# Kernel tuning notes

Measured on AMD Instinct MI355X. Metric: run time of the kernel, lower is better.

Reference implementation:

```python
import jax, jax.numpy as jnp
import numpy as np

B, P, D = 8, 1024, 768
H = 12
HD = D // H


def setup_inputs() -> dict:
    key = jax.random.key(0)
    k1, k2, k3, k4, k5 = jax.random.split(key, 5)
    s = 0.02
    return {
        "x": jax.random.normal(k1, (B, P, D), dtype=jnp.float32),
        "w_qkv": jax.random.normal(k2, (D, 3 * D), dtype=jnp.float32) * s,
        "b_qkv": jax.random.normal(k3, (3 * D,), dtype=jnp.float32) * s,
        "w_proj": jax.random.normal(k4, (D, D), dtype=jnp.float32) * s,
        "b_proj": jax.random.normal(k5, (D,), dtype=jnp.float32) * s,
    }


def reference(x, w_qkv, b_qkv, w_proj, b_proj):
    b, p, d = x.shape
    scale = HD ** -0.5
    qkv = x @ w_qkv + b_qkv                      # [B,P,3D]
    qkv = qkv.reshape(b, p, 3, H, HD).transpose(2, 0, 3, 1, 4)  # [3,B,H,P,HD]
    q, k, v = qkv[0], qkv[1], qkv[2]
    attn = jnp.einsum("bhqd,bhkd->bhqk", q, k) * scale
    attn = jax.nn.softmax(attn, axis=-1)         # attn_drop is identity (p=0)
    weighted_avg = jnp.einsum("bhqk,bhkd->bhqd", attn, v)
    weighted_avg = weighted_avg.transpose(0, 2, 1, 3).reshape(b, p, d)  # [B,P,D]
    out = weighted_avg @ w_proj + b_proj         # proj_drop is identity (p=0)
    return (out, weighted_avg)
```

## Files before the change

### kernel.cpp

```cpp
#include <hip/hip_runtime.h>
#include <hip/hip_bf16.h>


typedef __attribute__((ext_vector_type(8))) short short8;
typedef __attribute__((ext_vector_type(4))) float f32x4;

#define MFMA_BF16(a, b, c) __builtin_amdgcn_mfma_f32_16x16x32_bf16((a), (b), (c), 0, 0, 0)

#define NB 8
#define NP 1024
#define ND 768
#define NH 12
#define NHD 64
#define NTOK (NB * NP)
#define N3D (3 * ND)
#define OUT_HALF (NTOK * ND)
#define QSCALE 0.18033688f

__device__ __forceinline__ void gload_lds16(const void* gptr, void* ldsptr) {
  __builtin_amdgcn_global_load_lds(
      (const __attribute__((address_space(1))) unsigned int*)gptr,
      (__attribute__((address_space(3))) unsigned int*)ldsptr, 16, 0, 0);
}

__device__ __forceinline__ unsigned pack_bf16x2(float a, float b) {
  __hip_bfloat162 h = __float22bfloat162_rn(float2{a, b});
  return *reinterpret_cast<unsigned*>(&h);
}

__device__ __forceinline__ int swz_g(int b) { return b ^ (((b >> 7) & 7) << 4); }


__global__ void k_cvt_x(const float* __restrict__ in, __hip_bfloat16* __restrict__ out) {
  int i = (blockIdx.x * 256 + threadIdx.x) * 8;
  float4 a = *(const float4*)(in + i);
  float4 b = *(const float4*)(in + i + 4);
  union { __hip_bfloat16 h[8]; uint4 u; } r;
  r.h[0] = __float2bfloat16(a.x); r.h[1] = __float2bfloat16(a.y);
  r.h[2] = __float2bfloat16(a.z); r.h[3] = __float2bfloat16(a.w);
  r.h[4] = __float2bfloat16(b.x); r.h[5] = __float2bfloat16(b.y);
  r.h[6] = __float2bfloat16(b.z); r.h[7] = __float2bfloat16(b.w);
  *(uint4*)(out + i) = r.u;
}

__global__ void k_cvt_t(const float* __restrict__ in, __hip_bfloat16* __restrict__ out,
                        int K, int N) {
  __shared__ float tile[32][33];
  int k0 = blockIdx.x * 32;
  int n0 = blockIdx.y * 32;
  int r = threadIdx.x >> 5;
  int c = threadIdx.x & 31;
#pragma unroll
  for (int i = 0; i < 4; ++i)
    tile[r + 8 * i][c] = in[(size_t)(k0 + r + 8 * i) * N + n0 + c];
  __syncthreads();
#pragma unroll
  for (int i = 0; i < 4; ++i)
    out[(size_t)(n0 + r + 8 * i) * K + k0 + c] = __float2bfloat16(tile[c][r + 8 * i]);
}


__device__ __forceinline__ void gemm_mainloop(const __hip_bfloat16* __restrict__ A,
                                              const __hip_bfloat16* __restrict__ BT,
                                              int m0, int n0, char* Ls,
                                              f32x4 acc[4][4]) {
  const int tid = threadIdx.x;
  const int wid = tid >> 6, lane = tid & 63;
  const int wm = wid >> 1, wn = wid & 1;
  const int lrow = lane & 15, lk = lane >> 4;
  constexpr int K = 768, NKT = K / 32;

  int aoff[4], boff[4];
#pragma unroll
  for (int i = 0; i < 4; ++i) {
    aoff[i] = swz_g((wm * 64 + i * 16 + lrow) * 64 + lk * 16);
    boff[i] = swz_g((wn * 64 + i * 16 + lrow) * 64 + lk * 16);
  }

#define STAGE_G(kt, bi)                                                  \
  {                                                                      \
    const int k0s = (kt) * 32;                                           \
    char* dst = Ls + (bi) * 16384;                                       \
    _Pragma("unroll")                                                    \
    for (int t = 0; t < 2; ++t) {                                        \
      const int L = (tid + t * 256) * 16;          \
      const int lb = swz_g(L);              \
      const int mr = lb >> 6;                   \
      const int kk = (lb & 63) >> 1;            \
      gload_lds16(A + (size_t)(m0 + mr) * K + k0s + kk,                  \
                  dst + wid * 1024 + t * 4096);                          \
      gload_lds16(BT + (size_t)(n0 + mr) * K + k0s + kk,                 \
                  dst + 8192 + wid * 1024 + t * 4096);                   \
    }                                                                    \
  }

#define COMPUTE_T(kt)                                                          \
  {                                                                            \
    const char* buf = Ls + ((kt) % 3) * 16384;                                 \
    short8 af[4], bf[4];                                                       \
    _Pragma("unroll")                                                          \
    for (int i = 0; i < 4; ++i) {                                              \
      af[i] = *(const short8*)(buf + aoff[i]);                                 \
      bf[i] = *(const short8*)(buf + 8192 + boff[i]);                          \
    }                                                                          \
    _Pragma("unroll")                                                          \
    for (int mi = 0; mi < 4; ++mi)                                             \
      _Pragma("unroll")                                                        \
      for (int ni = 0; ni < 4; ++ni)                                           \
        acc[mi][ni] = MFMA_BF16(af[mi], bf[ni], acc[mi][ni]);                  \
  }

  STAGE_G(0, 0);
  STAGE_G(1, 1);

#pragma unroll 3
  for (int kt = 0; kt < NKT - 1; ++kt) {
    asm volatile("s_waitcnt vmcnt(4)" ::: "memory");
    __builtin_amdgcn_s_barrier();
    if (kt + 2 < NKT) STAGE_G(kt + 2, (kt + 2) % 3);
    COMPUTE_T(kt);
  }
  asm volatile("s_waitcnt vmcnt(0)" ::: "memory");
  __builtin_amdgcn_s_barrier();
  COMPUTE_T(NKT - 1);

#undef STAGE_G
#undef COMPUTE_T
}


__launch_bounds__(256)
__global__ void k_qkv_gemm(const __hip_bfloat16* __restrict__ A,
                           const __hip_bfloat16* __restrict__ BT,
                           const float* __restrict__ bias,
                           __hip_bfloat16* __restrict__ q_ws,
                           __hip_bfloat16* __restrict__ k_ws,
                           __hip_bfloat16* __restrict__ v_ws) {
  __shared__ char Ls[3 * 16384];
  const int mt = blockIdx.x & 63, nt = blockIdx.x >> 6;
  const int m0 = mt * 128, n0 = nt * 128;
  const int wid = threadIdx.x >> 6, lane = threadIdx.x & 63;
  const int wm = wid >> 1, wn = wid & 1;
  const int lrow = lane & 15, lk = lane >> 4;

  f32x4 acc[4][4] = {};
  gemm_mainloop(A, BT, m0, n0, Ls, acc);

  const int which = n0 / ND;
#pragma unroll
  for (int ni = 0; ni < 4; ++ni) {
    const int n = n0 + wn * 64 + ni * 16 + lrow;
    const float bv = bias[n];
    const int hh = (n % ND) >> 6;
    const int hd = n & 63;
#pragma unroll
    for (int mi = 0; mi < 4; ++mi) {
      const int mbase = m0 + wm * 64 + mi * 16 + lk * 4;
#pragma unroll
      for (int i = 0; i < 4; ++i) {
        const int m = mbase + i;
        const float v = acc[mi][ni][i] + bv;
        const int b = m >> 10, p = m & 1023;
        const int bh = b * NH + hh;
        if (which == 0)      q_ws[((size_t)bh * NP + p) * NHD + hd] = __float2bfloat16(v * QSCALE);
        else if (which == 1) k_ws[((size_t)bh * NP + p) * NHD + hd] = __float2bfloat16(v);
        else                 v_ws[((size_t)bh * NHD + hd) * NP + p] = __float2bfloat16(v);
      }
    }
  }
}


#define KVBLK 64

__launch_bounds__(256)
__global__ void k_attn(const __hip_bfloat16* __restrict__ q_ws,
                       const __hip_bfloat16* __restrict__ k_ws,
                       const __hip_bfloat16* __restrict__ v_ws,
                       float* __restrict__ wavg_f32,
                       __hip_bfloat16* __restrict__ wavg_bf) {
  __shared__ char smem[2 * 16384 + 4 * 2304];
  const int bh = blockIdx.y;
  const int tid = threadIdx.x;
  const int wid = tid >> 6, lane = tid & 63;
  const int lrow = lane & 15, lk = lane >> 4;
  const int q0 = blockIdx.x * 64 + wid * 16;
  char* pbuf = smem + 32768 + wid * 2304;

  const __hip_bfloat16* Qb = q_ws + (size_t)bh * NP * NHD;
  const __hip_bfloat16* Kb = k_ws + (size_t)bh * NP * NHD;
  const __hip_bfloat16* Vb = v_ws + (size_t)bh * NHD * NP;

  short8 qf0 = *(const short8*)(Qb + (size_t)(q0 + lrow) * NHD + lk * 8);
  short8 qf1 = *(const short8*)(Qb + (size_t)(q0 + lrow) * NHD + 32 + lk * 8);

  f32x4 acc[4] = {};
  float dsa = 0.f, dsb = 0.f;

#define STAGE(buf, key0)                                                          \
  {                                                                               \
    _Pragma("unroll")                                                             \
    for (int p = 0; p < 2; ++p) {                                                 \
      const int L = p * 4096 + tid * 16;                                          \
      const int r = L >> 7;                                                       \
      const int cb = L & 127;                                                     \
      const int sc = (cb ^ ((r & 7) << 4)) >> 1;        \
      gload_lds16(Kb + (size_t)((key0) + r) * NHD + sc, (buf) + L);               \
      gload_lds16(Vb + (size_t)r * NP + (key0) + sc, (buf) + 8192 + L);           \
    }                                                                             \
  }

  char* cur = smem;
  char* nxt = smem + 16384;
  STAGE(cur, 0);
  __syncthreads();

  for (int kc = 0; kc < NP / KVBLK; ++kc) {
    if (kc < NP / KVBLK - 1) STAGE(nxt, (kc + 1) * KVBLK);

    char* Ks = cur;
    char* Vs = cur + 8192;

    f32x4 s[4];
#pragma unroll
    for (int kt = 0; kt < 4; ++kt) {
      const int row = kt * 16 + lrow;
      const int sw = (row & 7) << 4;
      short8 klo = *(const short8*)(Ks + row * 128 + ((lk * 16) ^ sw));
      short8 khi = *(const short8*)(Ks + row * 128 + ((64 + lk * 16) ^ sw));
      f32x4 z = {0.f, 0.f, 0.f, 0.f};
      s[kt] = MFMA_BF16(klo, qf0, z);
      s[kt] = MFMA_BF16(khi, qf1, s[kt]);
    }

#pragma unroll
    for (int kt = 0; kt < 4; ++kt) {
      const float p0 = __builtin_amdgcn_exp2f(s[kt][0]);
      const float p1 = __builtin_amdgcn_exp2f(s[kt][1]);
      const float p2 = __builtin_amdgcn_exp2f(s[kt][2]);
      const float p3 = __builtin_amdgcn_exp2f(s[kt][3]);
      dsa += p0 + p1;
      dsb += p2 + p3;
      uint2 w;
      w.x = pack_bf16x2(p0, p1);
      w.y = pack_bf16x2(p2, p3);
      *(uint2*)(pbuf + lrow * 144 + kt * 32 + lk * 8) = w;
    }

#pragma unroll
    for (int kh = 0; kh < 2; ++kh) {
      short8 a2 = *(const short8*)(pbuf + lrow * 144 + kh * 64 + lk * 16);
#pragma unroll
      for (int hdt = 0; hdt < 4; ++hdt) {
        const int row = hdt * 16 + lrow;
        short8 vf = *(const short8*)(Vs + row * 128 +
                                     ((kh * 64 + lk * 16) ^ ((row & 7) << 4)));
        acc[hdt] = MFMA_BF16(a2, vf, acc[hdt]);
      }
    }

    __syncthreads();
    char* t = cur; cur = nxt; nxt = t;
  }

  float ds = dsa + dsb;
  ds += __shfl_xor(ds, 16);
  ds += __shfl_xor(ds, 32);
  float rd[4];
#pragma unroll
  for (int i = 0; i < 4; ++i) rd[i] = 1.0f / __shfl(ds, lk * 4 + i, 16);

  const int b = bh / NH, hh = bh % NH;
#pragma unroll
  for (int hdt = 0; hdt < 4; ++hdt) {
#pragma unroll
    for (int i = 0; i < 4; ++i) {
      const int qq = q0 + lk * 4 + i;
      const int col = hh * NHD + hdt * 16 + lrow;
      const float val = acc[hdt][i] * rd[i];
      const size_t o = ((size_t)b * NP + qq) * ND + col;
      wavg_f32[o] = val;
      wavg_bf[o] = __float2bfloat16(val);
    }
  }
#undef STAGE
}


__launch_bounds__(256)
__global__ void k_proj_gemm(const __hip_bfloat16* __restrict__ A,
                            const __hip_bfloat16* __restrict__ BT,
                            const float* __restrict__ bias,
                            float* __restrict__ C) {
  __shared__ char Ls[3 * 16384];
  const int mt = blockIdx.x & 63, nt = blockIdx.x >> 6;
  const int m0 = mt * 128, n0 = nt * 128;
  const int wid = threadIdx.x >> 6, lane = threadIdx.x & 63;
  const int wm = wid >> 1, wn = wid & 1;
  const int lrow = lane & 15, lk = lane >> 4;

  f32x4 acc[4][4] = {};
  gemm_mainloop(A, BT, m0, n0, Ls, acc);

#pragma unroll
  for (int ni = 0; ni < 4; ++ni) {
    const int n = n0 + wn * 64 + ni * 16 + lrow;
    const float bv = bias[n];
#pragma unroll
    for (int mi = 0; mi < 4; ++mi) {
      const int mbase = m0 + wm * 64 + mi * 16 + lk * 4;
#pragma unroll
      for (int i = 0; i < 4; ++i)
        C[(size_t)(mbase + i) * ND + n] = acc[mi][ni][i] + bv;
    }
  }
}


extern "C" void kernel_launch(void* const* d_in, const int* in_sizes, int n_in,
                              void* d_out, int out_size, void* d_ws, size_t ws_size,
                              hipStream_t stream) {
  const float* x      = (const float*)d_in[0];
  const float* w_qkv  = (const float*)d_in[1];
  const float* b_qkv  = (const float*)d_in[2];
  const float* w_proj = (const float*)d_in[3];
  const float* b_proj = (const float*)d_in[4];
  float* out = (float*)d_out;
  float* wavg_out = out + OUT_HALF;

  char* ws = (char*)d_ws;
  __hip_bfloat16* xbf    = (__hip_bfloat16*)(ws);
  __hip_bfloat16* wqkvT  = (__hip_bfloat16*)(ws + 12582912);
  __hip_bfloat16* wprojT = (__hip_bfloat16*)(ws + 16121856);
  __hip_bfloat16* q_ws   = (__hip_bfloat16*)(ws + 17301504);
  __hip_bfloat16* k_ws   = (__hip_bfloat16*)(ws + 29884416);
  __hip_bfloat16* v_ws   = (__hip_bfloat16*)(ws + 42467328);
  __hip_bfloat16* wavg_bf = xbf;

  k_cvt_x<<<NTOK * ND / (256 * 8), 256, 0, stream>>>(x, xbf);
  k_cvt_t<<<dim3(ND / 32, N3D / 32), 256, 0, stream>>>(w_qkv, wqkvT, ND, N3D);
  k_cvt_t<<<dim3(ND / 32, ND / 32), 256, 0, stream>>>(w_proj, wprojT, ND, ND);
  k_qkv_gemm<<<(NTOK / 128) * (N3D / 128), 256, 0, stream>>>(xbf, wqkvT, b_qkv,
                                                             q_ws, k_ws, v_ws);
  k_attn<<<dim3(NP / 64, NB * NH), 256, 0, stream>>>(q_ws, k_ws, v_ws, wavg_out, wavg_bf);
  k_proj_gemm<<<(NTOK / 128) * (ND / 128), 256, 0, stream>>>(wavg_bf, wprojT, b_proj, out);
}
```

Measured before the change: 132.9 us.

## Process 32 queries per wave in attention and swizzle block mapping

Each wave in the attention kernel now computes two 16-row query groups, reusing each K and V fragment loaded from LDS for twice the MFMA work and halving the number of blocks that stream K/V. Block IDs are remapped so consecutive blocks spread across heads and query tiles, and MFMA sections get raised wave priority. Register use and LDS for the P buffer both double, which may reduce occupancy.

Result: no change. 130.7 us (-1.7%).

```diff
diff --git a/kernel.cpp b/kernel.cpp
--- a/kernel.cpp
+++ b/kernel.cpp
@@ -179,23 +179,29 @@
                        const __hip_bfloat16* __restrict__ v_ws,
                        float* __restrict__ wavg_f32,
                        __hip_bfloat16* __restrict__ wavg_bf) {
-  __shared__ char smem[2 * 16384 + 4 * 2304];
-  const int bh = blockIdx.y;
+  __shared__ char smem[2 * 16384 + 4 * 4608];
+  const int bid = blockIdx.x;
+  const int wg = (bid & 7) * 96 + (bid >> 3);
+  const int bh = wg >> 3, qb = wg & 7;
   const int tid = threadIdx.x;
   const int wid = tid >> 6, lane = tid & 63;
   const int lrow = lane & 15, lk = lane >> 4;
-  const int q0 = blockIdx.x * 64 + wid * 16;
-  char* pbuf = smem + 32768 + wid * 2304;
+  const int q0 = qb * 128 + wid * 32;
+  char* pbuf = smem + 32768 + wid * 4608;
 
   const __hip_bfloat16* Qb = q_ws + (size_t)bh * NP * NHD;
   const __hip_bfloat16* Kb = k_ws + (size_t)bh * NP * NHD;
   const __hip_bfloat16* Vb = v_ws + (size_t)bh * NHD * NP;
 
-  short8 qf0 = *(const short8*)(Qb + (size_t)(q0 + lrow) * NHD + lk * 8);
-  short8 qf1 = *(const short8*)(Qb + (size_t)(q0 + lrow) * NHD + 32 + lk * 8);
-
-  f32x4 acc[4] = {};
-  float dsa = 0.f, dsb = 0.f;
+  short8 qf[2][2];
+#pragma unroll
+  for (int g = 0; g < 2; ++g) {
+    qf[g][0] = *(const short8*)(Qb + (size_t)(q0 + g * 16 + lrow) * NHD + lk * 8);
+    qf[g][1] = *(const short8*)(Qb + (size_t)(q0 + g * 16 + lrow) * NHD + 32 + lk * 8);
+  }
+
+  f32x4 acc[2][4] = {};
+  float dsum[2] = {0.f, 0.f};
 
 #define STAGE(buf, key0)                                                          \
   {                                                                               \
@@ -221,7 +227,8 @@
     char* Ks = cur;
     char* Vs = cur + 8192;
 
-    f32x4 s[4];
+    f32x4 s[2][4];
+    __builtin_amdgcn_s_setprio(1);
 #pragma unroll
     for (int kt = 0; kt < 4; ++kt) {
       const int row = kt * 16 + lrow;
@@ -229,58 +236,69 @@
       short8 klo = *(const short8*)(Ks + row * 128 + ((lk * 16) ^ sw));
       short8 khi = *(const short8*)(Ks + row * 128 + ((64 + lk * 16) ^ sw));
       f32x4 z = {0.f, 0.f, 0.f, 0.f};
-      s[kt] = MFMA_BF16(klo, qf0, z);
-      s[kt] = MFMA_BF16(khi, qf1, s[kt]);
-    }
-
-#pragma unroll
-    for (int kt = 0; kt < 4; ++kt) {
-      const float p0 = __builtin_amdgcn_exp2f(s[kt][0]);
-      const float p1 = __builtin_amdgcn_exp2f(s[kt][1]);
-      const float p2 = __builtin_amdgcn_exp2f(s[kt][2]);
-      const float p3 = __builtin_amdgcn_exp2f(s[kt][3]);
-      dsa += p0 + p1;
-      dsb += p2 + p3;
-      uint2 w;
-      w.x = pack_bf16x2(p0, p1);
-      w.y = pack_bf16x2(p2, p3);
-      *(uint2*)(pbuf + lrow * 144 + kt * 32 + lk * 8) = w;
-    }
-
+      s[0][kt] = MFMA_BF16(klo, qf[0][0], z);
+      s[0][kt] = MFMA_BF16(khi, qf[0][1], s[0][kt]);
+      s[1][kt] = MFMA_BF16(klo, qf[1][0], z);
+      s[1][kt] = MFMA_BF16(khi, qf[1][1], s[1][kt]);
+    }
+    __builtin_amdgcn_s_setprio(0);
+
+#pragma unroll
+    for (int g = 0; g < 2; ++g)
+#pragma unroll
+      for (int kt = 0; kt < 4; ++kt) {
+        const float p0 = __builtin_amdgcn_exp2f(s[g][kt][0]);
+        const float p1 = __builtin_amdgcn_exp2f(s[g][kt][1]);
+        const float p2 = __builtin_amdgcn_exp2f(s[g][kt][2]);
+        const float p3 = __builtin_amdgcn_exp2f(s[g][kt][3]);
+        dsum[g] += (p0 + p1) + (p2 + p3);
+        uint2 w;
+        w.x = pack_bf16x2(p0, p1);
+        w.y = pack_bf16x2(p2, p3);
+        *(uint2*)(pbuf + (g * 16 + lrow) * 144 + kt * 32 + lk * 8) = w;
+      }
+
+    __builtin_amdgcn_s_setprio(1);
 #pragma unroll
     for (int kh = 0; kh < 2; ++kh) {
-      short8 a2 = *(const short8*)(pbuf + lrow * 144 + kh * 64 + lk * 16);
+      short8 a20 = *(const short8*)(pbuf + lrow * 144 + kh * 64 + lk * 16);
+      short8 a21 = *(const short8*)(pbuf + (16 + lrow) * 144 + kh * 64 + lk * 16);
 #pragma unroll
       for (int hdt = 0; hdt < 4; ++hdt) {
         const int row = hdt * 16 + lrow;
         short8 vf = *(const short8*)(Vs + row * 128 +
                                      ((kh * 64 + lk * 16) ^ ((row & 7) << 4)));
-        acc[hdt] = MFMA_BF16(a2, vf, acc[hdt]);
+        acc[0][hdt] = MFMA_BF16(a20, vf, acc[0][hdt]);
+        acc[1][hdt] = MFMA_BF16(a21, vf, acc[1][hdt]);
       }
     }
+    __builtin_amdgcn_s_setprio(0);
 
     __syncthreads();
     char* t = cur; cur = nxt; nxt = t;
   }
 
-  float ds = dsa + dsb;
-  ds += __shfl_xor(ds, 16);
-  ds += __shfl_xor(ds, 32);
-  float rd[4];
-#pragma unroll
-  for (int i = 0; i < 4; ++i) rd[i] = 1.0f / __shfl(ds, lk * 4 + i, 16);
-
   const int b = bh / NH, hh = bh % NH;
 #pragma unroll
-  for (int hdt = 0; hdt < 4; ++hdt) {
-#pragma unroll
-    for (int i = 0; i < 4; ++i) {
-      const int qq = q0 + lk * 4 + i;
-      const int col = hh * NHD + hdt * 16 + lrow;
-      const float val = acc[hdt][i] * rd[i];
-      const size_t o = ((size_t)b * NP + qq) * ND + col;
-      wavg_f32[o] = val;
-      wavg_bf[o] = __float2bfloat16(val);
+  for (int g = 0; g < 2; ++g) {
+    float ds = dsum[g];
+    ds += __shfl_xor(ds, 16);
+    ds += __shfl_xor(ds, 32);
+    float rd[4];
+#pragma unroll
+    for (int i = 0; i < 4; ++i) rd[i] = 1.0f / __shfl(ds, lk * 4 + i, 16);
+
+#pragma unroll
+    for (int hdt = 0; hdt < 4; ++hdt) {
+#pragma unroll
+      for (int i = 0; i < 4; ++i) {
+        const int qq = q0 + g * 16 + lk * 4 + i;
+        const int col = hh * NHD + hdt * 16 + lrow;
+        const float val = acc[g][hdt][i] * rd[i];
+        const size_t o = ((size_t)b * NP + qq) * ND + col;
+        wavg_f32[o] = val;
+        wavg_bf[o] = __float2bfloat16(val);
+      }
     }
   }
 #undef STAGE
@@ -342,6 +360,6 @@
   k_cvt_t<<<dim3(ND / 32, ND / 32), 256, 0, stream>>>(w_proj, wprojT, ND, ND);
   k_qkv_gemm<<<(NTOK / 128) * (N3D / 128), 256, 0, stream>>>(xbf, wqkvT, b_qkv,
                                                              q_ws, k_ws, v_ws);
-  k_attn<<<dim3(NP / 64, NB * NH), 256, 0, stream>>>(q_ws, k_ws, v_ws, wavg_out, wavg_bf);
+  k_attn<<<(NP / 128) * (NB * NH), 256, 0, stream>>>(q_ws, k_ws, v_ws, wavg_out, wavg_bf);
   k_proj_gemm<<<(NTOK / 128) * (ND / 128), 256, 0, stream>>>(wavg_bf, wprojT, b_proj, out);
 }
```
